# Kernel tuning notes

Measured on AMD Instinct MI355X. Metric: run time of the kernel, lower is better.

The kernel has to match this reference:

```python
import jax, jax.numpy as jnp
import numpy as np

B, N, E, L, H, D = 16, 128, 2048, 4, 8, 64


def setup_inputs() -> dict:
    key = jax.random.key(0)
    k1, k2, k3, k4, k5 = jax.random.split(key, 5)
    edge_feat = jax.random.normal(k1, (B, E, D), dtype=jnp.float32)
    # index E (== num edges) is the zero-feature padding slot
    path_idx = jax.random.randint(k2, (B, N, N, L), 0, E + 1).astype(jnp.int32)
    dist = jax.random.randint(k3, (B, N, N), 0, L + 1).astype(jnp.int32)
    node_counts = jax.random.randint(k4, (B,), N // 2, N + 1).astype(jnp.int32)
    emb_table = jax.random.normal(k5, (L * H, D), dtype=jnp.float32)
    return {"edge_feat": edge_feat, "path_idx": path_idx, "dist": dist,
            "node_counts": node_counts, "emb_table": emb_table}


def reference(edge_feat, path_idx, dist, node_counts, emb_table):
    b, e, d = edge_feat.shape
    n = path_idx.shape[1]
    l = path_idx.shape[-1]
    h = emb_table.shape[0] // l
    # append zero row so padding index e gathers zeros (torch: cat zeros row)
    edata = jnp.concatenate([edge_feat, jnp.zeros((b, 1, d), edge_feat.dtype)], axis=1)
    # ragged per-graph path gather, batched: (b, n, n, l, d)
    path_data = jax.vmap(lambda ef, p: ef[p])(edata, path_idx)
    # embedding_idx = arange(h*l).reshape(l, h) -> table rows reshape to (l, h, d)
    emb = emb_table.reshape(l, h, d)
    # torch: einsum('xyld,dlh->xyh') with emb permuted (d,l,h); equivalent here
    enc = jnp.einsum('bxyld,lhd->bxyh', path_data, emb)
    dist_c = jnp.clip(dist, 1, l).astype(enc.dtype)  # clamp(min=1, max=path_len)
    enc = enc / dist_c[..., None]
    ar = jnp.arange(n)
    valid = (ar[None, :, None] < node_counts[:, None, None]) & \
            (ar[None, None, :] < node_counts[:, None, None])  # (b, n, n)
    neg_inf = jnp.asarray(-jnp.inf, enc.dtype)
    return jnp.where(valid[..., None], enc, neg_inf)
```

## Files before the change

kernel.cpp:

```cpp
#include <hip/hip_runtime.h>
#include <hip/hip_bf16.h>
#include <math.h>

#define BB 16
#define NN 128
#define EE 2048
#define LL 4
#define HH 8
#define DD 64
#define LH 32

#define NEG_SENTINEL (-1.0e30f)

__global__ __launch_bounds__(256) void precompute_proj(
    const float* __restrict__ edge_feat,
    const float* __restrict__ emb,
    float* __restrict__ proj)
{
    const int lane = threadIdx.x & 63;
    const int wave = threadIdx.x >> 6;
    const int wave_global = blockIdx.x * 4 + wave;
    const int row0 = wave_global * 4;

    float emb_r[LH];
#pragma unroll
    for (int j = 0; j < LH; ++j) emb_r[j] = emb[j * DD + lane];

    const int l5 = lane & 31;
    const int jrev = ((l5 & 1) << 4) | ((l5 & 2) << 2) | (l5 & 4) |
                     ((l5 & 8) >> 2) | ((l5 & 16) >> 4);

    for (int r = 0; r < 4; ++r) {
        const int row = row0 + r;
        const float ef = edge_feat[row * DD + lane];

        float acc[LH];
#pragma unroll
        for (int j = 0; j < LH; ++j) acc[j] = ef * emb_r[j];

#pragma unroll
        for (int s = 0; s < 5; ++s) {
            const int o = 1 << s;
            const int m = 32 >> s;
            const bool hi = (lane & o) != 0;
#pragma unroll
            for (int i = 0; i < (m >> 1); ++i) {
                float a = acc[i];
                float bv = acc[i + (m >> 1)];
                float send = hi ? a : bv;
                float recv = __shfl_xor(send, o, 64);
                acc[i] = (hi ? bv : a) + recv;
            }
        }
        const float total = acc[0] + __shfl_xor(acc[0], 32, 64);

        if (lane < 32) {
            proj[row * LH + jrev] = total;
        }
    }
}

__global__ __launch_bounds__(256) void path_gather(
    const int* __restrict__ path_idx,
    const int* __restrict__ dist,
    const int* __restrict__ node_counts,
    const float* __restrict__ proj,
    __hip_bfloat16* __restrict__ out)
{
    const int tid = blockIdx.x * blockDim.x + threadIdx.x;
    const int h   = tid & 7;
    const int pos = tid >> 3;
    const int y   = pos & (NN - 1);
    const int x   = (pos >> 7) & (NN - 1);
    const int b   = pos >> 14;

    const int4 idx4 = ((const int4*)path_idx)[pos];
    const int  dv   = dist[pos];
    const int  nc   = node_counts[b];

    const float* pb = proj + (size_t)b * EE * LH;

    const int i0 = idx4.x, i1 = idx4.y, i2 = idx4.z, i3 = idx4.w;
    const float v0 = pb[min(i0, EE - 1) * LH + 0 * HH + h];
    const float v1 = pb[min(i1, EE - 1) * LH + 1 * HH + h];
    const float v2 = pb[min(i2, EE - 1) * LH + 2 * HH + h];
    const float v3 = pb[min(i3, EE - 1) * LH + 3 * HH + h];

    float s = (i0 < EE ? v0 : 0.f) + (i1 < EE ? v1 : 0.f) +
              (i2 < EE ? v2 : 0.f) + (i3 < EE ? v3 : 0.f);

    int dc = dv < 1 ? 1 : (dv > LL ? LL : dv);
    float r = s / (float)dc;

    const bool valid = (x < nc) && (y < nc);
    out[tid] = __float2bfloat16(valid ? r : NEG_SENTINEL);
}

extern "C" void kernel_launch(void* const* d_in, const int* in_sizes, int n_in,
                              void* d_out, int out_size, void* d_ws, size_t ws_size,
                              hipStream_t stream) {
    const float* edge_feat   = (const float*)d_in[0];
    const int*   path_idx    = (const int*)d_in[1];
    const int*   dist        = (const int*)d_in[2];
    const int*   node_counts = (const int*)d_in[3];
    const float* emb_table   = (const float*)d_in[4];
    __hip_bfloat16* out = (__hip_bfloat16*)d_out;

    float* proj = (float*)d_ws;

    precompute_proj<<<2048, 256, 0, stream>>>(edge_feat, emb_table, proj);

    path_gather<<<8192, 256, 0, stream>>>(path_idx, dist, node_counts, proj, out);
}
```

Measured before the change: 88.87 us.

## Store projections in bf16 and process all heads per thread with vector loads

```diff
diff --git a/kernel.cpp b/kernel.cpp
--- a/kernel.cpp
+++ b/kernel.cpp
@@ -15,7 +15,7 @@
 __global__ __launch_bounds__(256) void precompute_proj(
     const float* __restrict__ edge_feat,
     const float* __restrict__ emb,
-    float* __restrict__ proj)
+    __hip_bfloat16* __restrict__ proj)
 {
     const int lane = threadIdx.x & 63;
     const int wave = threadIdx.x >> 6;
@@ -55,7 +55,7 @@
         const float total = acc[0] + __shfl_xor(acc[0], 32, 64);
 
         if (lane < 32) {
-            proj[row * LH + jrev] = total;
+            proj[row * LH + jrev] = __float2bfloat16(total);
         }
     }
 }
@@ -64,12 +64,10 @@
     const int* __restrict__ path_idx,
     const int* __restrict__ dist,
     const int* __restrict__ node_counts,
-    const float* __restrict__ proj,
+    const __hip_bfloat16* __restrict__ proj,
     __hip_bfloat16* __restrict__ out)
 {
-    const int tid = blockIdx.x * blockDim.x + threadIdx.x;
-    const int h   = tid & 7;
-    const int pos = tid >> 3;
+    const int pos = blockIdx.x * blockDim.x + threadIdx.x;
     const int y   = pos & (NN - 1);
     const int x   = (pos >> 7) & (NN - 1);
     const int b   = pos >> 14;
@@ -78,22 +76,42 @@
     const int  dv   = dist[pos];
     const int  nc   = node_counts[b];
 
-    const float* pb = proj + (size_t)b * EE * LH;
+    const uint4* pb = (const uint4*)(proj + (size_t)b * EE * LH);
 
-    const int i0 = idx4.x, i1 = idx4.y, i2 = idx4.z, i3 = idx4.w;
-    const float v0 = pb[min(i0, EE - 1) * LH + 0 * HH + h];
-    const float v1 = pb[min(i1, EE - 1) * LH + 1 * HH + h];
-    const float v2 = pb[min(i2, EE - 1) * LH + 2 * HH + h];
-    const float v3 = pb[min(i3, EE - 1) * LH + 3 * HH + h];
+    const int idx[4] = {idx4.x, idx4.y, idx4.z, idx4.w};
+    float s[HH];
+#pragma unroll
+    for (int h = 0; h < HH; ++h) s[h] = 0.f;
 
-    float s = (i0 < EE ? v0 : 0.f) + (i1 < EE ? v1 : 0.f) +
-              (i2 < EE ? v2 : 0.f) + (i3 < EE ? v3 : 0.f);
+#pragma unroll
+    for (int l = 0; l < LL; ++l) {
+        const int  ii    = idx[l];
+        const bool live  = (ii < EE);
+        uint4 v = pb[min(ii, EE - 1) * 4 + l];
+        if (!live) { v.x = 0u; v.y = 0u; v.z = 0u; v.w = 0u; }
+        const unsigned u[4] = {v.x, v.y, v.z, v.w};
+#pragma unroll
+        for (int p = 0; p < 4; ++p) {
+            float flo = __uint_as_float(u[p] << 16);
+            float fhi = __uint_as_float(u[p] & 0xFFFF0000u);
+            s[2 * p + 0] += flo;
+            s[2 * p + 1] += fhi;
+        }
+    }
 
-    int dc = dv < 1 ? 1 : (dv > LL ? LL : dv);
-    float r = s / (float)dc;
+    const int   dc = dv < 1 ? 1 : (dv > LL ? LL : dv);
+    const float rd = 1.0f / (float)dc;
+    const bool valid = (x < nc) && (y < nc);
 
-    const bool valid = (x < nc) && (y < nc);
-    out[tid] = __float2bfloat16(valid ? r : NEG_SENTINEL);
+    uint4 ov;
+    unsigned short* po = (unsigned short*)&ov;
+#pragma unroll
+    for (int h = 0; h < HH; ++h) {
+        const float r = valid ? s[h] * rd : NEG_SENTINEL;
+        __hip_bfloat16 bh = __float2bfloat16(r);
+        po[h] = *(unsigned short*)&bh;
+    }
+    ((uint4*)out)[pos] = ov;
 }
 
 extern "C" void kernel_launch(void* const* d_in, const int* in_sizes, int n_in,
@@ -106,9 +124,9 @@
     const float* emb_table   = (const float*)d_in[4];
     __hip_bfloat16* out = (__hip_bfloat16*)d_out;
 
-    float* proj = (float*)d_ws;
+    __hip_bfloat16* proj = (__hip_bfloat16*)d_ws;
 
     precompute_proj<<<2048, 256, 0, stream>>>(edge_feat, emb_table, proj);
 
-    path_gather<<<8192, 256, 0, stream>>>(path_idx, dist, node_counts, proj, out);
+    path_gather<<<1024, 256, 0, stream>>>(path_idx, dist, node_counts, proj, out);
 }
```

Result: no change. 88.52 us (-0.4%).
